# Optimization experiments

Hardware: AMD Instinct MI355X
Metric: run time of the kernel (lower is better)

The kernel has to match this reference:

```python
import jax, jax.numpy as jnp
import numpy as np

N = 4194304  # data_size
EPS = 1e-12  # torch f.normalize eps


def setup_inputs() -> dict:
    key = jax.random.key(0)
    k1, = jax.random.split(key, 1)
    inputs = jax.random.normal(k1, (N, 3, 3), dtype=jnp.float32)
    kd = jnp.zeros((3,), dtype=jnp.float32)   # nn.Parameter([0,0,0])
    ks = jnp.ones((3,), dtype=jnp.float32)    # nn.Parameter([1,1,1])
    p = jnp.float32(16.0)                     # nn.Parameter(16.0)
    return {"inputs": inputs, "kd": kd, "ks": ks, "p": p}


def reference(inputs, kd, ks, p):
    # inputs: [N, 3, 3] -> light, normal, view each [N, 3]
    light = inputs[:, 0, :]
    normal = inputs[:, 1, :]
    view = inputs[:, 2, :]
    intensity = jnp.float32(1.0)

    # diffuse: kd * intensity * max(0, dot(light, normal))  -> [N, 1] * [3]
    ln = jnp.maximum(0.0, jnp.sum(light * normal, axis=-1, keepdims=True))
    l_d = kd * intensity * ln  # [N, 3]

    # half vector: normalize(light + view) with torch's eps clamp on norm
    h = light + view
    norm = jnp.maximum(jnp.linalg.norm(h, axis=-1, keepdims=True), EPS)
    half = h / norm

    # specular: ks * intensity * max(0, dot(normal, half)) ** p
    nh = jnp.maximum(0.0, jnp.sum(normal * half, axis=-1, keepdims=True))
    l_s = ks * intensity * jnp.power(nh, p)  # [N, 3]

    return l_s + l_d  # [N, 3]
```

## Files before the change

kernel.cpp:

```cpp
#include <hip/hip_runtime.h>
#include <math.h>


#define BLOCK 256
#define EPT 4
#define TILE (BLOCK * EPT)

__global__ __launch_bounds__(BLOCK) void blinn_phong_kernel(
    const float* __restrict__ in,
    const float* __restrict__ kd,
    const float* __restrict__ ks,
    const float* __restrict__ pp,
    float* __restrict__ out,
    int n)
{
    __shared__ float s_mem[TILE * 9];

    const int tid = threadIdx.x;
    const long long blk0 = (long long)blockIdx.x * TILE;

    const float4* gin = (const float4*)(in + blk0 * 9);
    float4* s4 = (float4*)s_mem;
    const long long total4 = ((long long)n * 9) >> 2;
    const long long base4 = blk0 * 9 / 4;
    float4 r[9];
#pragma unroll
    for (int i = 0; i < 9; ++i) {
        if (base4 + tid + i * BLOCK < total4) r[i] = gin[tid + i * BLOCK];
    }
#pragma unroll
    for (int i = 0; i < 9; ++i) s4[tid + i * BLOCK] = r[i];
    __syncthreads();

    const float kd0 = kd[0], kd1 = kd[1], kd2 = kd[2];
    const float ks0 = ks[0], ks1 = ks[1], ks2 = ks[2];
    const float p = pp[0];

    float o[EPT][3];
#pragma unroll
    for (int m = 0; m < EPT; ++m) {
        const int j = tid + m * BLOCK;
        const float* e = s_mem + j * 9;
        float Lx = e[0], Ly = e[1], Lz = e[2];
        float Nx = e[3], Ny = e[4], Nz = e[5];
        float Vx = e[6], Vy = e[7], Vz = e[8];

        float ln = fmaxf(0.0f, Lx * Nx + Ly * Ny + Lz * Nz);

        float hx = Lx + Vx, hy = Ly + Vy, hz = Lz + Vz;
        float hh = hx * hx + hy * hy + hz * hz;
        float inv = rsqrtf(fmaxf(hh, 1e-24f));

        float nh = fmaxf(0.0f, (Nx * hx + Ny * hy + Nz * hz) * inv);
        float spec = __builtin_amdgcn_exp2f(p * __builtin_amdgcn_logf(nh));

        o[m][0] = ks0 * spec + kd0 * ln;
        o[m][1] = ks1 * spec + kd1 * ln;
        o[m][2] = ks2 * spec + kd2 * ln;
    }
    __syncthreads();

#pragma unroll
    for (int m = 0; m < EPT; ++m) {
        const int j = tid + m * BLOCK;
        s_mem[3 * j + 0] = o[m][0];
        s_mem[3 * j + 1] = o[m][1];
        s_mem[3 * j + 2] = o[m][2];
    }
    __syncthreads();

    float4* gout = (float4*)(out + blk0 * 3);
    const long long out_total4 = ((long long)n * 3) >> 2;
    const long long out_base4 = blk0 * 3 / 4;
#pragma unroll
    for (int m = 0; m < 3; ++m) {
        if (out_base4 + tid + m * BLOCK < out_total4)
            gout[tid + m * BLOCK] = s4[tid + m * BLOCK];
    }
}

extern "C" void kernel_launch(void* const* d_in, const int* in_sizes, int n_in,
                              void* d_out, int out_size, void* d_ws, size_t ws_size,
                              hipStream_t stream) {
    const float* in = (const float*)d_in[0];
    const float* kd = (const float*)d_in[1];
    const float* ks = (const float*)d_in[2];
    const float* pp = (const float*)d_in[3];
    float* out = (float*)d_out;

    int n = in_sizes[0] / 9;
    int grid = (n + TILE - 1) / TILE;
    blinn_phong_kernel<<<grid, BLOCK, 0, stream>>>(in, kd, ks, pp, out, n);
}
```

Measured before the change: 261.8 us.

## Drop LDS staging; each thread loads its own contiguous 4 elements directly

Removes the shared-memory transpose and its three barriers. Each thread now reads 9 consecutive float4s covering its 4 elements and writes 3 consecutive float4s. This saves LDS traffic and synchronisation, but global accesses become strided across lanes (144-byte stride per lane), which can hurt coalescing. It also drops the tail bounds checks, so it relies on n being a multiple of EPT.

```diff
diff --git a/kernel.cpp b/kernel.cpp
--- a/kernel.cpp
+++ b/kernel.cpp
@@ -4,7 +4,6 @@
 
 #define BLOCK 256
 #define EPT 4
-#define TILE (BLOCK * EPT)
 
 __global__ __launch_bounds__(BLOCK) void blinn_phong_kernel(
     const float* __restrict__ in,
@@ -14,69 +13,49 @@
     float* __restrict__ out,
     int n)
 {
-    __shared__ float s_mem[TILE * 9];
+    const long long g = (long long)blockIdx.x * BLOCK + threadIdx.x;
+    const long long e0 = g * EPT;
+    if (e0 >= n) return;
 
-    const int tid = threadIdx.x;
-    const long long blk0 = (long long)blockIdx.x * TILE;
+    const float4* __restrict__ gin4 = (const float4*)in;
+    float4* __restrict__ gout4 = (float4*)out;
 
-    const float4* gin = (const float4*)(in + blk0 * 9);
-    float4* s4 = (float4*)s_mem;
-    const long long total4 = ((long long)n * 9) >> 2;
-    const long long base4 = blk0 * 9 / 4;
     float4 r[9];
+    const long long ib = g * 9;
 #pragma unroll
-    for (int i = 0; i < 9; ++i) {
-        if (base4 + tid + i * BLOCK < total4) r[i] = gin[tid + i * BLOCK];
-    }
-#pragma unroll
-    for (int i = 0; i < 9; ++i) s4[tid + i * BLOCK] = r[i];
-    __syncthreads();
+    for (int i = 0; i < 9; ++i) r[i] = gin4[ib + i];
+    const float* f = (const float*)r;
 
     const float kd0 = kd[0], kd1 = kd[1], kd2 = kd[2];
     const float ks0 = ks[0], ks1 = ks[1], ks2 = ks[2];
     const float p = pp[0];
 
-    float o[EPT][3];
-#pragma unroll
-    for (int m = 0; m < EPT; ++m) {
-        const int j = tid + m * BLOCK;
-        const float* e = s_mem + j * 9;
-        float Lx = e[0], Ly = e[1], Lz = e[2];
-        float Nx = e[3], Ny = e[4], Nz = e[5];
-        float Vx = e[6], Vy = e[7], Vz = e[8];
-
-        float ln = fmaxf(0.0f, Lx * Nx + Ly * Ny + Lz * Nz);
-
-        float hx = Lx + Vx, hy = Ly + Vy, hz = Lz + Vz;
-        float hh = hx * hx + hy * hy + hz * hz;
-        float inv = rsqrtf(fmaxf(hh, 1e-24f));
-
-        float nh = fmaxf(0.0f, (Nx * hx + Ny * hy + Nz * hz) * inv);
-        float spec = __builtin_amdgcn_exp2f(p * __builtin_amdgcn_logf(nh));
-
-        o[m][0] = ks0 * spec + kd0 * ln;
-        o[m][1] = ks1 * spec + kd1 * ln;
-        o[m][2] = ks2 * spec + kd2 * ln;
-    }
-    __syncthreads();
+    float4 o[3];
+    float* ov = (float*)o;
 
 #pragma unroll
     for (int m = 0; m < EPT; ++m) {
-        const int j = tid + m * BLOCK;
-        s_mem[3 * j + 0] = o[m][0];
-        s_mem[3 * j + 1] = o[m][1];
-        s_mem[3 * j + 2] = o[m][2];
+        const float Lx = f[9*m+0], Ly = f[9*m+1], Lz = f[9*m+2];
+        const float Nx = f[9*m+3], Ny = f[9*m+4], Nz = f[9*m+5];
+        const float Vx = f[9*m+6], Vy = f[9*m+7], Vz = f[9*m+8];
+
+        const float ln = fmaxf(0.0f, Lx * Nx + Ly * Ny + Lz * Nz);
+
+        const float hx = Lx + Vx, hy = Ly + Vy, hz = Lz + Vz;
+        const float hh = hx * hx + hy * hy + hz * hz;
+        const float inv = rsqrtf(fmaxf(hh, 1e-24f));
+
+        const float nh = fmaxf(0.0f, (Nx * hx + Ny * hy + Nz * hz) * inv);
+        const float spec = __builtin_amdgcn_exp2f(p * __builtin_amdgcn_logf(nh));
+
+        ov[3*m + 0] = ks0 * spec + kd0 * ln;
+        ov[3*m + 1] = ks1 * spec + kd1 * ln;
+        ov[3*m + 2] = ks2 * spec + kd2 * ln;
     }
-    __syncthreads();
 
-    float4* gout = (float4*)(out + blk0 * 3);
-    const long long out_total4 = ((long long)n * 3) >> 2;
-    const long long out_base4 = blk0 * 3 / 4;
+    const long long ob = g * 3;
 #pragma unroll
-    for (int m = 0; m < 3; ++m) {
-        if (out_base4 + tid + m * BLOCK < out_total4)
-            gout[tid + m * BLOCK] = s4[tid + m * BLOCK];
-    }
+    for (int m = 0; m < 3; ++m) gout4[ob + m] = o[m];
 }
 
 extern "C" void kernel_launch(void* const* d_in, const int* in_sizes, int n_in,
@@ -89,6 +68,7 @@
     float* out = (float*)d_out;
 
     int n = in_sizes[0] / 9;
-    int grid = (n + TILE - 1) / TILE;
+    int threads_needed = (n + EPT - 1) / EPT;
+    int grid = (threads_needed + BLOCK - 1) / BLOCK;
     blinn_phong_kernel<<<grid, BLOCK, 0, stream>>>(in, kd, ks, pp, out, n);
 }
```

Measured after the change: 229.7 us. 1.14x faster.
